# Performance work log

Measured on AMD Instinct MI355X. Metric: run time of the kernel, lower is better.

The kernel has to match this reference:

```python
import jax, jax.numpy as jnp
import numpy as np

N_NODES = 50000
N_EDGES = 500000
D = 128
K_CLUSTERS = 1024  # fixed cluster count for Kongming_Cluster
EPS = 1e-8


def setup_inputs() -> dict:
    key = jax.random.key(0)
    k1, k2, k3, k4 = jax.random.split(key, 4)
    x = jax.random.normal(k1, (N_NODES, D), dtype=jnp.float32)
    edge_index = jax.random.randint(k2, (2, N_EDGES), 0, N_NODES, dtype=jnp.int32)
    W1 = jax.random.normal(k3, (D, D), dtype=jnp.float32) * (1.0 / np.sqrt(D))
    b1 = jax.random.normal(k4, (D,), dtype=jnp.float32) * 0.01
    return {"x": x, "edge_index": edge_index, "W1": W1, "b1": b1}


def reference(x, edge_index, W1, b1):
    src, dst = edge_index[0], edge_index[1]
    # --- SLPropagate: mean aggregation of neighbor features over edge list ---
    msg = x[src]                                               # [E, D] gather
    agg = jax.ops.segment_sum(msg, dst, num_segments=N_NODES)  # [N, D] scatter-add
    deg = jax.ops.segment_sum(jnp.ones((N_EDGES,), x.dtype), dst, num_segments=N_NODES)
    h = agg / jnp.maximum(deg, 1.0)[:, None]                   # [N, D]

    # --- Kongming_Cluster: cosine-similarity assignment to K centroids ---
    hn = h / (jnp.linalg.norm(h, axis=-1, keepdims=True) + EPS)  # row-normalized
    centroids = hn[:K_CLUSTERS]                                  # [K, D]
    sim = hn @ centroids.T                                       # [N, K] cosine sims
    assign = jnp.argmax(sim, axis=-1)                            # [N] cluster index
    counts = jax.ops.segment_sum(jnp.ones((N_NODES,), x.dtype), assign,
                                 num_segments=K_CLUSTERS)
    xc = jax.ops.segment_sum(h, assign, num_segments=K_CLUSTERS)
    xc = xc / jnp.maximum(counts, 1.0)[:, None]                  # [K, D] cluster means

    # --- lin1 on compressed representation ---
    y = xc @ W1.T + b1                                           # [K, D]

    # --- Kongming_Reconstruct: scatter/gather back to per-node rows ---
    out = y[assign]                                              # [N, D]
    return out
```

## Files before the change

### kernel.cpp

```cpp
#include <hip/hip_runtime.h>

#define N_NODES 50000
#define N_EDGES 500000
#define DIM 128
#define KC 1024
#define CAP 64
#define EPSV 1e-8f
#define LO_SCALE 4096.0f
#define INV_LO_SCALE (1.0f / 4096.0f)

typedef _Float16 f16x8 __attribute__((ext_vector_type(8)));
typedef _Float16 f16x4 __attribute__((ext_vector_type(4)));
typedef _Float16 f16x2 __attribute__((ext_vector_type(2)));
typedef float f32x4 __attribute__((ext_vector_type(4)));

__global__ void fill_buckets_k(const int* __restrict__ ei, int* __restrict__ bucket,
                               int* __restrict__ cursor) {
    int e = blockIdx.x * blockDim.x + threadIdx.x;
    if (e >= N_EDGES) return;
    int src = ei[e];
    int dst = ei[N_EDGES + e];
    int pos = atomicAdd(cursor + dst, 1);
    if (pos < CAP) bucket[dst * CAP + pos] = src;
}

__global__ void agg_norm_k(const float* __restrict__ x, const int* __restrict__ bucket,
                           const int* __restrict__ cursor, float* __restrict__ h,
                           _Float16* __restrict__ Ahi, _Float16* __restrict__ Alo) {
    const int lane = threadIdx.x & 63;
    const int wv = threadIdx.x >> 6;
    const int half = lane >> 5, q = lane & 31;
    const int n = blockIdx.x * 8 + wv * 2 + half;

    int cnt_mine = cursor[n];
    if (cnt_mine > CAP) cnt_mine = CAP;
    int cnt_other = __shfl_xor(cnt_mine, 32);
    int cmax = max(cnt_mine, cnt_other);

    if (cmax <= 32) {
        int v = (q < cnt_mine) ? bucket[n * CAP + q] : 0x7fffffff;
#pragma unroll
        for (int k = 2; k <= 32; k <<= 1) {
#pragma unroll
            for (int j = k >> 1; j >= 1; j >>= 1) {
                int other = __shfl_xor(v, j);
                bool lower = ((q & j) == 0);
                bool asc = ((q & k) == 0);
                int mn = min(v, other), mx = max(v, other);
                v = (lower == asc) ? mn : mx;
            }
        }
        const float4* x4p = (const float4*)x;
        float4 a4 = make_float4(0.f, 0.f, 0.f, 0.f);
        const int base = half << 5;
        for (int j = 0; j < cmax; j += 2) {
            int s0 = __shfl(v, base + j);
            int s1 = __shfl(v, base + j + 1);
            if (j < cnt_mine) {
                float4 t = x4p[(size_t)s0 * 32 + q];
                a4.x += t.x; a4.y += t.y; a4.z += t.z; a4.w += t.w;
            }
            if (j + 1 < cnt_mine) {
                float4 t = x4p[(size_t)s1 * 32 + q];
                a4.x += t.x; a4.y += t.y; a4.z += t.z; a4.w += t.w;
            }
        }
        float inv = 1.0f / (float)(cnt_mine > 0 ? cnt_mine : 1);
        float4 h4;
        h4.x = a4.x * inv; h4.y = a4.y * inv; h4.z = a4.z * inv; h4.w = a4.w * inv;
        float ss = h4.x * h4.x + h4.y * h4.y + h4.z * h4.z + h4.w * h4.w;
#pragma unroll
        for (int o = 1; o < 32; o <<= 1) ss += __shfl_xor(ss, o);
        float sc = 1.0f / (sqrtf(ss) + EPSV);
        float4 hn4;
        hn4.x = h4.x * sc; hn4.y = h4.y * sc; hn4.z = h4.z * sc; hn4.w = h4.w * sc;

        ((float4*)h)[(size_t)n * 32 + q] = h4;
        _Float16 h0 = (_Float16)hn4.x, h1 = (_Float16)hn4.y;
        _Float16 h2 = (_Float16)hn4.z, h3 = (_Float16)hn4.w;
        f16x4 ph = {h0, h1, h2, h3};
        f16x4 pl = {(_Float16)((hn4.x - (float)h0) * LO_SCALE),
                    (_Float16)((hn4.y - (float)h1) * LO_SCALE),
                    (_Float16)((hn4.z - (float)h2) * LO_SCALE),
                    (_Float16)((hn4.w - (float)h3) * LO_SCALE)};
        *(f16x4*)(Ahi + (size_t)n * DIM + q * 4) = ph;
        *(f16x4*)(Alo + (size_t)n * DIM + q * 4) = pl;
    } else {
        for (int tt = 0; tt < 2; ++tt) {
            int nn = blockIdx.x * 8 + wv * 2 + tt;
            int cnt = cursor[nn];
            if (cnt > CAP) cnt = CAP;
            int v = (lane < cnt) ? bucket[nn * CAP + lane] : 0x7fffffff;
#pragma unroll
            for (int k = 2; k <= 64; k <<= 1) {
#pragma unroll
                for (int j = k >> 1; j >= 1; j >>= 1) {
                    int other = __shfl_xor(v, j);
                    bool lower = ((lane & j) == 0);
                    bool asc = ((lane & k) == 0);
                    int mn = min(v, other), mx = max(v, other);
                    v = (lower == asc) ? mn : mx;
                }
            }
            const float2* x2 = (const float2*)x;
            float ax = 0.f, ay = 0.f;
            for (int j = 0; j < cnt; ++j) {
                int s = __shfl(v, j);
                float2 t = x2[(size_t)s * 64 + lane];
                ax += t.x; ay += t.y;
            }
            float degf = (float)(cnt > 0 ? cnt : 1);
            float hx = ax / degf, hy = ay / degf;
            float ss = hx * hx + hy * hy;
#pragma unroll
            for (int o = 1; o < 64; o <<= 1) ss += __shfl_xor(ss, o);
            float denom = sqrtf(ss) + EPSV;
            float hnx = hx / denom, hny = hy / denom;
            ((float2*)h)[(size_t)nn * 64 + lane] = make_float2(hx, hy);
            _Float16 hix = (_Float16)hnx, hiy = (_Float16)hny;
            f16x2 ph; ph[0] = hix; ph[1] = hiy;
            f16x2 pl; pl[0] = (_Float16)((hnx - (float)hix) * LO_SCALE);
            pl[1] = (_Float16)((hny - (float)hiy) * LO_SCALE);
            *(f16x2*)(Ahi + (size_t)nn * DIM + lane * 2) = ph;
            *(f16x2*)(Alo + (size_t)nn * DIM + lane * 2) = pl;
        }
    }
}

#define SWZ14(u) ((u) ^ ((((u) >> 8) & 7) << 4))

__global__ __launch_bounds__(256, 3) void sim_mfma3_k(const _Float16* __restrict__ Ahi,
                                                      const _Float16* __restrict__ Alo,
                                                      int* __restrict__ assign,
                                                      int* __restrict__ counts) {
    __shared__ __align__(16) char Bs[2][16384];
    const int lane = threadIdx.x & 63;
    const int wv = threadIdx.x >> 6;
    const int r16 = lane & 15, kg = lane >> 4;
    const int m0 = blockIdx.x * 128 + wv * 32;

    int ar0 = m0 + r16;      if (ar0 > N_NODES - 1) ar0 = N_NODES - 1;
    int ar1 = m0 + 16 + r16; if (ar1 > N_NODES - 1) ar1 = N_NODES - 1;
    f16x8 ah0[4], al0[4], ah1[4], al1[4];
#pragma unroll
    for (int ks = 0; ks < 4; ++ks) {
        size_t o0 = (size_t)ar0 * DIM + ks * 32 + kg * 8;
        size_t o1 = (size_t)ar1 * DIM + ks * 32 + kg * 8;
        ah0[ks] = *(const f16x8*)(Ahi + o0);
        al0[ks] = *(const f16x8*)(Alo + o0);
        ah1[ks] = *(const f16x8*)(Ahi + o1);
        al1[ks] = *(const f16x8*)(Alo + o1);
    }

    const int u0 = wv * 2048 + lane * 16;
    const int u1 = u0 + 1024;
    const int d0 = SWZ14(u0), d1 = SWZ14(u1);
    const int e0 = u0 >> 1, e1 = u1 >> 1;

    float best0_0 = -1e30f, best0_1 = -1e30f, best0_2 = -1e30f, best0_3 = -1e30f;
    float best1_0 = -1e30f, best1_1 = -1e30f, best1_2 = -1e30f, best1_3 = -1e30f;
    int bi0_0 = 0, bi0_1 = 0, bi0_2 = 0, bi0_3 = 0;
    int bi1_0 = 0, bi1_1 = 0, bi1_2 = 0, bi1_3 = 0;

    const int rbase = r16 * 256;
    const int x4 = (r16 & 7) << 4;

    f16x8 sA = *(const f16x8*)(Ahi + e0);
    f16x8 sB = *(const f16x8*)(Ahi + e1);
    f16x8 sC = *(const f16x8*)(Alo + e0);
    f16x8 sD = *(const f16x8*)(Alo + e1);
    {
        char* bc = &Bs[0][0];
        *(f16x8*)(bc + d0) = sA; *(f16x8*)(bc + d1) = sB;
        *(f16x8*)(bc + 8192 + d0) = sC; *(f16x8*)(bc + 8192 + d1) = sD;
    }
    __syncthreads();

    for (int kc = 0; kc < 32; ++kc) {
        const int cur = kc & 1;
        if (kc < 31) {
            int go = (kc + 1) * 4096;
            sA = *(const f16x8*)(Ahi + go + e0);
            sB = *(const f16x8*)(Ahi + go + e1);
            sC = *(const f16x8*)(Alo + go + e0);
            sD = *(const f16x8*)(Alo + go + e1);
        }
        char* bc = &Bs[cur][0];
#pragma unroll
        for (int ns = 0; ns < 2; ++ns) {
            f32x4 c1a = (f32x4){0.f, 0.f, 0.f, 0.f};
            f32x4 c2a = (f32x4){0.f, 0.f, 0.f, 0.f};
            f32x4 c1b = (f32x4){0.f, 0.f, 0.f, 0.f};
            f32x4 c2b = (f32x4){0.f, 0.f, 0.f, 0.f};
#pragma unroll
            for (int ks = 0; ks < 4; ++ks) {
                int off = ns * 4096 + rbase + ((ks * 64 + kg * 16) ^ x4);
                f16x8 bh = *(const f16x8*)(bc + off);
                f16x8 bl = *(const f16x8*)(bc + 8192 + off);
                c1a = __builtin_amdgcn_mfma_f32_16x16x32_f16(ah0[ks], bh, c1a, 0, 0, 0);
                c2a = __builtin_amdgcn_mfma_f32_16x16x32_f16(ah0[ks], bl, c2a, 0, 0, 0);
                c2a = __builtin_amdgcn_mfma_f32_16x16x32_f16(al0[ks], bh, c2a, 0, 0, 0);
                c1b = __builtin_amdgcn_mfma_f32_16x16x32_f16(ah1[ks], bh, c1b, 0, 0, 0);
                c2b = __builtin_amdgcn_mfma_f32_16x16x32_f16(ah1[ks], bl, c2b, 0, 0, 0);
                c2b = __builtin_amdgcn_mfma_f32_16x16x32_f16(al1[ks], bh, c2b, 0, 0, 0);
            }
            int col = kc * 32 + ns * 16 + r16;
            float s;
            s = c1a[0] + c2a[0] * INV_LO_SCALE; if (s > best0_0) { best0_0 = s; bi0_0 = col; }
            s = c1a[1] + c2a[1] * INV_LO_SCALE; if (s > best0_1) { best0_1 = s; bi0_1 = col; }
            s = c1a[2] + c2a[2] * INV_LO_SCALE; if (s > best0_2) { best0_2 = s; bi0_2 = col; }
            s = c1a[3] + c2a[3] * INV_LO_SCALE; if (s > best0_3) { best0_3 = s; bi0_3 = col; }
            s = c1b[0] + c2b[0] * INV_LO_SCALE; if (s > best1_0) { best1_0 = s; bi1_0 = col; }
            s = c1b[1] + c2b[1] * INV_LO_SCALE; if (s > best1_1) { best1_1 = s; bi1_1 = col; }
            s = c1b[2] + c2b[2] * INV_LO_SCALE; if (s > best1_2) { best1_2 = s; bi1_2 = col; }
            s = c1b[3] + c2b[3] * INV_LO_SCALE; if (s > best1_3) { best1_3 = s; bi1_3 = col; }
        }
        if (kc < 31) {
            char* bn = &Bs[cur ^ 1][0];
            *(f16x8*)(bn + d0) = sA; *(f16x8*)(bn + d1) = sB;
            *(f16x8*)(bn + 8192 + d0) = sC; *(f16x8*)(bn + 8192 + d1) = sD;
        }
        __syncthreads();
    }

    float bestA[8] = {best0_0, best0_1, best0_2, best0_3,
                      best1_0, best1_1, best1_2, best1_3};
    int bidxA[8] = {bi0_0, bi0_1, bi0_2, bi0_3, bi1_0, bi1_1, bi1_2, bi1_3};
#pragma unroll
    for (int qq = 0; qq < 8; ++qq) {
        float b = bestA[qq];
        int bi = bidxA[qq];
#pragma unroll
        for (int o = 1; o < 16; o <<= 1) {
            float os = __shfl_xor(b, o);
            int oi = __shfl_xor(bi, o);
            if (os > b || (os == b && oi < bi)) { b = os; bi = oi; }
        }
        if (r16 == 0) {
            int gr = m0 + (qq >> 2) * 16 + kg * 4 + (qq & 3);
            if (gr < N_NODES) {
                assign[gr] = bi;
                atomicAdd(counts + bi, 1);
            }
        }
    }
}

__global__ void scan_k(const int* __restrict__ counts, int* __restrict__ offs,
                       int* __restrict__ ccur) {
    __shared__ int buf[KC];
    int t = threadIdx.x;
    int v = counts[t];
    buf[t] = v;
    __syncthreads();
#pragma unroll
    for (int o = 1; o < KC; o <<= 1) {
        int u = (t >= o) ? buf[t - o] : 0;
        __syncthreads();
        buf[t] += u;
        __syncthreads();
    }
    int excl = buf[t] - v;
    offs[t] = excl;
    ccur[t] = excl;
}

__global__ void fill_clist_k(const int* __restrict__ assign, int* __restrict__ ccur,
                             int* __restrict__ clist) {
    int n = blockIdx.x * 256 + threadIdx.x;
    if (n >= N_NODES) return;
    int p = atomicAdd(ccur + assign[n], 1);
    clist[p] = n;
}

__global__ void xcy_k(const float* __restrict__ h, const int* __restrict__ clist,
                      const int* __restrict__ offs, const int* __restrict__ counts,
                      const float* __restrict__ W1, const float* __restrict__ b1,
                      float* __restrict__ y) {
    __shared__ float xr[DIM];
    int c = blockIdx.x, t = threadIdx.x;
    int s = offs[c], cnt = counts[c];
    float acc = 0.f;
    for (int i = 0; i < cnt; ++i) {
        int n = clist[s + i];
        acc += h[(size_t)n * DIM + t];
    }
    xr[t] = acc / (float)(cnt > 0 ? cnt : 1);
    __syncthreads();

    const float4* w4 = (const float4*)(W1 + t * DIM);
    float a0 = 0.f, a1 = 0.f, a2 = 0.f, a3 = 0.f;
#pragma unroll
    for (int kk = 0; kk < 32; ++kk) {
        float4 w = w4[kk];
        a0 = fmaf(xr[4 * kk + 0], w.x, a0);
        a1 = fmaf(xr[4 * kk + 1], w.y, a1);
        a2 = fmaf(xr[4 * kk + 2], w.z, a2);
        a3 = fmaf(xr[4 * kk + 3], w.w, a3);
    }
    y[c * DIM + t] = (a0 + a1) + (a2 + a3) + b1[t];
}

__global__ void scatter_out_k(const float* __restrict__ y, const int* __restrict__ assign,
                              float* __restrict__ out) {
    int i = blockIdx.x * blockDim.x + threadIdx.x;
    int n = i >> 5, q = i & 31;
    int a = assign[n];
    ((float4*)out)[(size_t)n * 32 + q] = ((const float4*)y)[a * 32 + q];
}

extern "C" void kernel_launch(void* const* d_in, const int* in_sizes, int n_in,
                              void* d_out, int out_size, void* d_ws, size_t ws_size,
                              hipStream_t stream) {
    const float* x  = (const float*)d_in[0];
    const int*   ei = (const int*)d_in[1];
    const float* W1 = (const float*)d_in[2];
    const float* b1 = (const float*)d_in[3];
    float* out = (float*)d_out;

    char* ws = (char*)d_ws;
    float* h      = (float*)(ws);
    int*   bucket = (int*)(ws + 25600000);
    int*   clist  = (int*)(ws + 25600000);
    int*   offs   = (int*)(ws + 25800000);
    int*   ccur   = (int*)(ws + 25804096);
    int*   cursor = (int*)(ws + 38400000);
    int*   counts = (int*)(ws + 38600000);
    int*   assign = (int*)(ws + 39128384);
    float* y      = (float*)(ws + 39328384);

    _Float16* Ahi = (_Float16*)d_out;
    _Float16* Alo = (_Float16*)((char*)d_out + 12800000);

    hipMemsetAsync(ws + 38400000, 0, 204096, stream);

    fill_buckets_k<<<(N_EDGES + 255) / 256, 256, 0, stream>>>(ei, bucket, cursor);
    agg_norm_k<<<N_NODES / 8, 256, 0, stream>>>(x, bucket, cursor, h, Ahi, Alo);
    sim_mfma3_k<<<(N_NODES + 127) / 128, 256, 0, stream>>>(Ahi, Alo, assign, counts);
    scan_k<<<1, KC, 0, stream>>>(counts, offs, ccur);
    fill_clist_k<<<(N_NODES + 255) / 256, 256, 0, stream>>>(assign, ccur, clist);
    xcy_k<<<KC, 128, 0, stream>>>(h, clist, offs, counts, W1, b1, y);
    scatter_out_k<<<(N_NODES * 32) / 256, 256, 0, stream>>>(y, assign, out);
}
```

Measured before the change: 179.7 us.

## Split similarity argmax across two centroid halves with packed 64-bit atomicMax

The similarity/argmax kernel now splits the 1024 centroids across a second grid dimension, so each block scans 512 centroids instead of all 1024. Partial results are merged with a 64-bit atomicMax on a key that packs the order-preserving float bits with the inverted index, which keeps the lowest index on ties. A new decode kernel then writes assign and the counts. This doubles the grid (391 to 782 blocks) to fill more CUs, at the cost of an extra memset, an extra small kernel launch, and each block reloading its A rows.

Result: slower. 191.4 us (+6.5%).

```diff
diff --git a/kernel.cpp b/kernel.cpp
--- a/kernel.cpp
+++ b/kernel.cpp
@@ -13,6 +13,11 @@
 typedef _Float16 f16x4 __attribute__((ext_vector_type(4)));
 typedef _Float16 f16x2 __attribute__((ext_vector_type(2)));
 typedef float f32x4 __attribute__((ext_vector_type(4)));
+
+__device__ __forceinline__ unsigned ford(float f) {
+    unsigned b = __float_as_uint(f);
+    return (b & 0x80000000u) ? ~b : (b | 0x80000000u);
+}
 
 __global__ void fill_buckets_k(const int* __restrict__ ei, int* __restrict__ bucket,
                                int* __restrict__ cursor) {
@@ -129,15 +134,16 @@
 
 #define SWZ14(u) ((u) ^ ((((u) >> 8) & 7) << 4))
 
-__global__ __launch_bounds__(256, 3) void sim_mfma3_k(const _Float16* __restrict__ Ahi,
+__global__ __launch_bounds__(256, 3) void sim_mfma4_k(const _Float16* __restrict__ Ahi,
                                                       const _Float16* __restrict__ Alo,
-                                                      int* __restrict__ assign,
-                                                      int* __restrict__ counts) {
+                                                      unsigned long long* __restrict__ keys) {
     __shared__ __align__(16) char Bs[2][16384];
     const int lane = threadIdx.x & 63;
     const int wv = threadIdx.x >> 6;
     const int r16 = lane & 15, kg = lane >> 4;
     const int m0 = blockIdx.x * 128 + wv * 32;
+    const int cbase = blockIdx.y * 65536;
+    const int col0 = blockIdx.y * 512;
 
     int ar0 = m0 + r16;      if (ar0 > N_NODES - 1) ar0 = N_NODES - 1;
     int ar1 = m0 + 16 + r16; if (ar1 > N_NODES - 1) ar1 = N_NODES - 1;
@@ -165,10 +171,10 @@
     const int rbase = r16 * 256;
     const int x4 = (r16 & 7) << 4;
 
-    f16x8 sA = *(const f16x8*)(Ahi + e0);
-    f16x8 sB = *(const f16x8*)(Ahi + e1);
-    f16x8 sC = *(const f16x8*)(Alo + e0);
-    f16x8 sD = *(const f16x8*)(Alo + e1);
+    f16x8 sA = *(const f16x8*)(Ahi + cbase + e0);
+    f16x8 sB = *(const f16x8*)(Ahi + cbase + e1);
+    f16x8 sC = *(const f16x8*)(Alo + cbase + e0);
+    f16x8 sD = *(const f16x8*)(Alo + cbase + e1);
     {
         char* bc = &Bs[0][0];
         *(f16x8*)(bc + d0) = sA; *(f16x8*)(bc + d1) = sB;
@@ -176,10 +182,10 @@
     }
     __syncthreads();
 
-    for (int kc = 0; kc < 32; ++kc) {
+    for (int kc = 0; kc < 16; ++kc) {
         const int cur = kc & 1;
-        if (kc < 31) {
-            int go = (kc + 1) * 4096;
+        if (kc < 15) {
+            int go = cbase + (kc + 1) * 4096;
             sA = *(const f16x8*)(Ahi + go + e0);
             sB = *(const f16x8*)(Ahi + go + e1);
             sC = *(const f16x8*)(Alo + go + e0);
@@ -204,7 +210,7 @@
                 c2b = __builtin_amdgcn_mfma_f32_16x16x32_f16(ah1[ks], bl, c2b, 0, 0, 0);
                 c2b = __builtin_amdgcn_mfma_f32_16x16x32_f16(al1[ks], bh, c2b, 0, 0, 0);
             }
-            int col = kc * 32 + ns * 16 + r16;
+            int col = col0 + kc * 32 + ns * 16 + r16;
             float s;
             s = c1a[0] + c2a[0] * INV_LO_SCALE; if (s > best0_0) { best0_0 = s; bi0_0 = col; }
             s = c1a[1] + c2a[1] * INV_LO_SCALE; if (s > best0_1) { best0_1 = s; bi0_1 = col; }
@@ -215,7 +221,7 @@
             s = c1b[2] + c2b[2] * INV_LO_SCALE; if (s > best1_2) { best1_2 = s; bi1_2 = col; }
             s = c1b[3] + c2b[3] * INV_LO_SCALE; if (s > best1_3) { best1_3 = s; bi1_3 = col; }
         }
-        if (kc < 31) {
+        if (kc < 15) {
             char* bn = &Bs[cur ^ 1][0];
             *(f16x8*)(bn + d0) = sA; *(f16x8*)(bn + d1) = sB;
             *(f16x8*)(bn + 8192 + d0) = sC; *(f16x8*)(bn + 8192 + d1) = sD;
@@ -239,11 +245,21 @@
         if (r16 == 0) {
             int gr = m0 + (qq >> 2) * 16 + kg * 4 + (qq & 3);
             if (gr < N_NODES) {
-                assign[gr] = bi;
-                atomicAdd(counts + bi, 1);
-            }
-        }
-    }
+                unsigned long long key =
+                    ((unsigned long long)ford(b) << 32) | (unsigned)(KC - 1 - bi);
+                atomicMax(keys + gr, key);
+            }
+        }
+    }
+}
+
+__global__ void decode_count_k(const unsigned long long* __restrict__ keys,
+                               int* __restrict__ assign, int* __restrict__ counts) {
+    int n = blockIdx.x * 256 + threadIdx.x;
+    if (n >= N_NODES) return;
+    int a = (KC - 1) - (int)(unsigned)(keys[n] & 0xFFFFFFFFull);
+    assign[n] = a;
+    atomicAdd(counts + a, 1);
 }
 
 __global__ void scan_k(const int* __restrict__ counts, int* __restrict__ offs,
@@ -324,6 +340,7 @@
     int*   clist  = (int*)(ws + 25600000);
     int*   offs   = (int*)(ws + 25800000);
     int*   ccur   = (int*)(ws + 25804096);
+    unsigned long long* keys = (unsigned long long*)(ws + 25808192);
     int*   cursor = (int*)(ws + 38400000);
     int*   counts = (int*)(ws + 38600000);
     int*   assign = (int*)(ws + 39128384);
@@ -336,7 +353,9 @@
 
     fill_buckets_k<<<(N_EDGES + 255) / 256, 256, 0, stream>>>(ei, bucket, cursor);
     agg_norm_k<<<N_NODES / 8, 256, 0, stream>>>(x, bucket, cursor, h, Ahi, Alo);
-    sim_mfma3_k<<<(N_NODES + 127) / 128, 256, 0, stream>>>(Ahi, Alo, assign, counts);
+    hipMemsetAsync(ws + 25808192, 0, N_NODES * 8, stream);
+    sim_mfma4_k<<<dim3((N_NODES + 127) / 128, 2), 256, 0, stream>>>(Ahi, Alo, keys);
+    decode_count_k<<<(N_NODES + 255) / 256, 256, 0, stream>>>(keys, assign, counts);
     scan_k<<<1, KC, 0, stream>>>(counts, offs, ccur);
     fill_clist_k<<<(N_NODES + 255) / 256, 256, 0, stream>>>(assign, ccur, clist);
     xcy_k<<<KC, 128, 0, stream>>>(h, clist, offs, counts, W1, b1, y);
```
